# Kernel tuning notes

Hardware: AMD Instinct MI355X
Metric: run time of the kernel (lower is better)

Reference implementation:

```python
import jax, jax.numpy as jnp
import numpy as np

EMBED_DIM = 1024
NUM_HEADS = 16
HEAD_DIM = EMBED_DIM // NUM_HEADS


def setup_inputs() -> dict:
    key = jax.random.key(0)
    k1, k2, k3, k4 = jax.random.split(key, 4)
    x = jax.random.normal(k1, (2, 2048, EMBED_DIM), dtype=jnp.float32)
    # nn.Linear weights: stored as [out, in]; we keep that convention.
    s = 1.0 / np.sqrt(EMBED_DIM)
    w_qkv = jax.random.uniform(k2, (3 * EMBED_DIM, EMBED_DIM), jnp.float32, -s, s)
    w_proj = jax.random.uniform(k3, (EMBED_DIM, EMBED_DIM), jnp.float32, -s, s)
    b_proj = jax.random.uniform(k4, (EMBED_DIM,), jnp.float32, -s, s)
    return {"x": x, "w_qkv": w_qkv, "w_proj": w_proj, "b_proj": b_proj}


def reference(x, w_qkv, w_proj, b_proj):
    B, N, C = x.shape
    H, D = NUM_HEADS, HEAD_DIM
    scale = D ** -0.5
    # qkv: [B, N, 3C] -> [3, B, H, N, D]
    qkv = jnp.einsum('bnc,oc->bno', x, w_qkv)
    qkv = qkv.reshape(B, N, 3, H, D).transpose(2, 0, 3, 1, 4)
    q, k, v = qkv[0] * scale, qkv[1], qkv[2]
    attn = jax.nn.softmax(jnp.einsum('bhnd,bhmd->bhnm', q, k), axis=-1)
    out = jnp.einsum('bhnm,bhmd->bhnd', attn, v)
    out = out.transpose(0, 2, 1, 3).reshape(B, N, C)
    return jnp.einsum('bnc,oc->bno', out, w_proj) + b_proj
```

## Files before the change

### kernel.cpp

```cpp
#include <hip/hip_runtime.h>


constexpr int B_ = 2, N_ = 2048, C_ = 1024, H_ = 16, D_ = 64;
constexpr int M_ = B_ * N_;
constexpr int O3 = 3 * C_;
constexpr int KVB = 64;
constexpr int NTILES = N_ / KVB;

typedef short bf16x8 __attribute__((ext_vector_type(8)));
typedef _Float16 half8 __attribute__((ext_vector_type(8)));
typedef _Float16 half4v __attribute__((ext_vector_type(4)));
typedef float f32x4  __attribute__((ext_vector_type(4)));
typedef float f32x16 __attribute__((ext_vector_type(16)));

__device__ __forceinline__ unsigned short f2bf(float f) {
    unsigned int u = __float_as_uint(f);
    unsigned int r = (u + 0x7FFFu + ((u >> 16) & 1u)) >> 16;
    return (unsigned short)r;
}

__device__ __forceinline__ float fexp2(float x) {
    return __builtin_amdgcn_exp2f(x);
}

__device__ __forceinline__ void async16(const void* g, void* l) {
    __builtin_amdgcn_global_load_lds(
        (const __attribute__((address_space(1))) unsigned int*)g,
        (__attribute__((address_space(3))) unsigned int*)l, 16, 0, 0);
}

constexpr size_t XN  = (size_t)M_ * C_;
constexpr size_t WQN = (size_t)O3 * C_;
constexpr size_t WPN = (size_t)C_ * C_;

__global__ __launch_bounds__(256)
void convert_f16(const float* __restrict__ x, const float* __restrict__ wq,
                 const float* __restrict__ wp, _Float16* __restrict__ dst)
{
    size_t i = ((size_t)blockIdx.x * 256 + threadIdx.x) * 8;
    const float* src;
    size_t off;
    if (i < XN)            { src = x;  off = i; }
    else if (i < XN + WQN) { src = wq; off = i - XN; }
    else                   { src = wp; off = i - XN - WQN; }
    float4 a = *(const float4*)(src + off);
    float4 b = *(const float4*)(src + off + 4);
    half8 h;
    h[0] = (_Float16)a.x; h[1] = (_Float16)a.y; h[2] = (_Float16)a.z; h[3] = (_Float16)a.w;
    h[4] = (_Float16)b.x; h[5] = (_Float16)b.y; h[6] = (_Float16)b.z; h[7] = (_Float16)b.w;
    *(half8*)(dst + i) = h;
}

template<int MODE>
__global__ __launch_bounds__(256)
void gemm128(const _Float16* __restrict__ Ag, const _Float16* __restrict__ Bg,
             unsigned short* __restrict__ Qd, unsigned short* __restrict__ Kd,
             unsigned short* __restrict__ Vt,
             const float* __restrict__ bias, float* __restrict__ Out)
{
    __shared__ __align__(16) unsigned char Ab[2][16384];
    __shared__ __align__(16) unsigned char Bb[2][16384];

    const int t    = threadIdx.x;
    const int lane = t & 63;
    const int w    = t >> 6;
    const int g    = lane >> 4;
    const int c    = lane & 15;
    const int wm   = w >> 1, wn = w & 1;
    const int bm   = blockIdx.y * 128;
    const int bn   = blockIdx.x * 128;
    constexpr int K = C_;

    f32x4 acc[4][4];
    f32x4 zero = {0.f, 0.f, 0.f, 0.f};
    #pragma unroll
    for (int mi = 0; mi < 4; ++mi)
        #pragma unroll
        for (int ni = 0; ni < 4; ++ni) acc[mi][ni] = zero;

    auto stage = [&](int buf, int k0) {
        #pragma unroll
        for (int i = 0; i < 4; ++i) {
            int id  = t + 256 * i;
            int row = id >> 3;
            int p   = id & 7;
            int gs  = p ^ (row & 7);
            async16(Ag + (size_t)(bm + row) * K + k0 + 8 * gs, &Ab[buf][id * 16]);
            async16(Bg + (size_t)(bn + row) * K + k0 + 8 * gs, &Bb[buf][id * 16]);
        }
    };

    stage(0, 0);
    __syncthreads();
    int cur = 0;

    for (int k0 = 0; k0 < K; k0 += 64) {
        if (k0 + 64 < K) stage(cur ^ 1, k0 + 64);

        const unsigned char* Abase = Ab[cur];
        const unsigned char* Bbase = Bb[cur];
        #pragma unroll
        for (int s = 0; s < 2; ++s) {
            half8 af[4], bf[4];
            #pragma unroll
            for (int mi = 0; mi < 4; ++mi) {
                int row = wm * 64 + mi * 16 + c;
                af[mi] = *(const half8*)(Abase + (row * 8 + ((s * 4 + g) ^ (row & 7))) * 16);
            }
            #pragma unroll
            for (int ni = 0; ni < 4; ++ni) {
                int row = wn * 64 + ni * 16 + c;
                bf[ni] = *(const half8*)(Bbase + (row * 8 + ((s * 4 + g) ^ (row & 7))) * 16);
            }
            #pragma unroll
            for (int mi = 0; mi < 4; ++mi)
                #pragma unroll
                for (int ni = 0; ni < 4; ++ni)
                    acc[mi][ni] = __builtin_amdgcn_mfma_f32_16x16x32_f16(af[mi], bf[ni], acc[mi][ni], 0, 0, 0);
        }

        __syncthreads();
        cur ^= 1;
    }

    if constexpr (MODE == 0) {
        constexpr float QSCALE = 0.125f * 1.4426950408889634f;
        const int o0 = bn + wn * 64;
        const int which = o0 >> 10;
        const int h  = (o0 & 1023) >> 6;
        const int m0 = bm + wm * 64;
        const int b  = m0 >> 11;
        const int n0 = m0 & 2047;
        const size_t bh = (size_t)b * H_ + h;
        if (which == 0) {
            unsigned short* base = Qd + (bh * N_) * D_;
            #pragma unroll
            for (int mi = 0; mi < 4; ++mi)
                #pragma unroll
                for (int ni = 0; ni < 4; ++ni)
                    #pragma unroll
                    for (int r = 0; r < 4; ++r)
                        base[(size_t)(n0 + mi * 16 + 4 * g + r) * D_ + ni * 16 + c] =
                            f2bf(acc[mi][ni][r] * QSCALE);
        } else if (which == 1) {
            unsigned short* base = Kd + (bh * N_) * D_;
            #pragma unroll
            for (int mi = 0; mi < 4; ++mi)
                #pragma unroll
                for (int ni = 0; ni < 4; ++ni)
                    #pragma unroll
                    for (int r = 0; r < 4; ++r)
                        base[(size_t)(n0 + mi * 16 + 4 * g + r) * D_ + ni * 16 + c] =
                            f2bf(acc[mi][ni][r]);
        } else {
            unsigned short* base = Vt + (bh * D_) * (size_t)N_;
            #pragma unroll
            for (int mi = 0; mi < 4; ++mi)
                #pragma unroll
                for (int ni = 0; ni < 4; ++ni) {
                    ushort4 v;
                    v.x = f2bf(acc[mi][ni][0]);
                    v.y = f2bf(acc[mi][ni][1]);
                    v.z = f2bf(acc[mi][ni][2]);
                    v.w = f2bf(acc[mi][ni][3]);
                    *(ushort4*)&base[(size_t)(ni * 16 + c) * N_ + n0 + mi * 16 + 4 * g] = v;
                }
        }
    } else {
        const int m0 = bm + wm * 64;
        const int o0 = bn + wn * 64;
        #pragma unroll
        for (int ni = 0; ni < 4; ++ni) {
            float bb = bias[o0 + ni * 16 + c];
            #pragma unroll
            for (int mi = 0; mi < 4; ++mi)
                #pragma unroll
                for (int r = 0; r < 4; ++r)
                    Out[(size_t)(m0 + mi * 16 + 4 * g + r) * C_ + o0 + ni * 16 + c] =
                        acc[mi][ni][r] + bb;
        }
    }
}

__global__ __launch_bounds__(512, 4)
void attn_mfma(const unsigned short* __restrict__ Qd, const unsigned short* __restrict__ Kd,
               const unsigned short* __restrict__ Vt, _Float16* __restrict__ AO)
{
    __shared__ __align__(16) unsigned char Kbuf[2][2][8192];
    __shared__ __align__(16) unsigned char Vbuf[2][2][8192];

    const int t    = threadIdx.x;
    const int lane = t & 63;
    const int w    = t >> 6;
    const int wg   = w >> 2;
    const int wl   = w & 3;
    const int tl   = t & 255;
    const int h    = lane >> 5;
    const int q31  = lane & 31;
    const int qsw  = q31 & 7;

    int flat = blockIdx.x;
    int work = (flat & 7) * 64 + (flat >> 3);
    const int bh = work >> 4;
    const int qt = work & 15;
    const int b  = bh >> 4, hh = bh & 15;
    const int q0 = qt * 128;

    const unsigned short* Kp = Kd + (size_t)bh * N_ * D_;
    const unsigned short* Vp = Vt + (size_t)bh * D_ * N_;

    const unsigned short* qp = Qd + ((size_t)bh * N_ + q0 + wl * 32 + q31) * D_;
    bf16x8 qf[4];
    #pragma unroll
    for (int s = 0; s < 4; ++s)
        qf[s] = *(const bf16x8*)(qp + 16 * s + 8 * h);

    int go[4];
    #pragma unroll
    for (int s = 0; s < 4; ++s) go[s] = ((2 * s + h) ^ qsw) << 4;
    const int row0off = q31 * 128;
    const int row1off = (32 + q31) * 128;

    const int rk = tl >> 3, pk = tl & 7;
    const unsigned char* kSrc = (const unsigned char*)Kp + rk * 128 + ((pk ^ (rk & 7)) << 4);
    const unsigned char* vSrc = (const unsigned char*)Vp + (size_t)rk * (N_ * 2) + ((pk ^ (rk & 7)) << 4);
    unsigned char* kDstA = Kbuf[wg][0] + tl * 16;
    unsigned char* kDstB = Kbuf[wg][1] + tl * 16;
    unsigned char* vDstA = Vbuf[wg][0] + tl * 16;
    unsigned char* vDstB = Vbuf[wg][1] + tl * 16;
    const unsigned char* kb0 = Kbuf[wg][0];
    const unsigned char* kb1 = Kbuf[wg][1];
    const unsigned char* vb0 = Vbuf[wg][0];
    const unsigned char* vb1 = Vbuf[wg][1];

    float l_run = 0.f;
    f32x16 oc0 = 0.f, oc1 = 0.f;

    auto stage = [&](unsigned char* kD, unsigned char* vD, int kt) {
        async16(kSrc + (size_t)kt * 8192, kD);
        async16(kSrc + (size_t)kt * 8192 + 4096, kD + 4096);
        async16(vSrc + (size_t)kt * 128, vD);
        async16(vSrc + 32 * (size_t)(N_ * 2) + (size_t)kt * 128, vD + 4096);
    };

    const int kt0 = wg * 16, ktEnd = kt0 + 16;
    stage(kDstA, vDstA, kt0);
    __syncthreads();

    auto tile_body = [&](const unsigned char* kbase, const unsigned char* vbase,
                         unsigned char* kDstN, unsigned char* vDstN, int ktNext) {
        if (ktNext < ktEnd) stage(kDstN, vDstN, ktNext);

        f32x16 st0 = 0.f, st1 = 0.f;
        const unsigned char* krow0 = kbase + row0off;
        const unsigned char* krow1 = kbase + row1off;
        __builtin_amdgcn_s_setprio(1);
        #pragma unroll
        for (int s = 0; s < 4; ++s) {
            bf16x8 a0 = *(const bf16x8*)(krow0 + go[s]);
            bf16x8 a1 = *(const bf16x8*)(krow1 + go[s]);
            st0 = __builtin_amdgcn_mfma_f32_32x32x16_bf16(a0, qf[s], st0, 0, 0, 0);
            st1 = __builtin_amdgcn_mfma_f32_32x32x16_bf16(a1, qf[s], st1, 0, 0, 0);
        }
        __builtin_amdgcn_s_setprio(0);

        #pragma unroll
        for (int r = 0; r < 16; ++r) {
            st0[r] = fexp2(st0[r]);
            st1[r] = fexp2(st1[r]);
        }

        f32x16 sv = st0 + st1;
        float ts = ((sv[0] + sv[1]) + (sv[2] + sv[3])) + ((sv[4] + sv[5]) + (sv[6] + sv[7]))
                 + ((sv[8] + sv[9]) + (sv[10] + sv[11])) + ((sv[12] + sv[13]) + (sv[14] + sv[15]));
        l_run += ts;

        unsigned int pkd[2][4][2];
        #pragma unroll
        for (int m = 0; m < 4; ++m)
            #pragma unroll
            for (int j = 0; j < 2; ++j) {
                pkd[0][m][j] = __byte_perm(__float_as_uint(st0[4*m + 2*j]),
                                           __float_as_uint(st0[4*m + 2*j + 1]), 0x7632);
                pkd[1][m][j] = __byte_perm(__float_as_uint(st1[4*m + 2*j]),
                                           __float_as_uint(st1[4*m + 2*j + 1]), 0x7632);
            }

        #pragma unroll
        for (int kb = 0; kb < 2; ++kb)
            #pragma unroll
            for (int u = 0; u < 2; ++u)
                #pragma unroll
                for (int j = 0; j < 2; ++j)
                    asm("v_permlane32_swap_b32 %0, %1"
                        : "+v"(pkd[kb][2*u][j]), "+v"(pkd[kb][2*u+1][j]));

        bf16x8 pb[4];
        #pragma unroll
        for (int s = 0; s < 4; ++s) {
            const int kb = s >> 1, u = s & 1;
            union { unsigned int d[4]; bf16x8 v; } uu;
            uu.d[0] = pkd[kb][2*u][0];
            uu.d[1] = pkd[kb][2*u][1];
            uu.d[2] = pkd[kb][2*u+1][0];
            uu.d[3] = pkd[kb][2*u+1][1];
            pb[s] = uu.v;
        }

        const unsigned char* vrow0 = vbase + row0off;
        const unsigned char* vrow1 = vbase + row1off;
        __builtin_amdgcn_s_setprio(1);
        #pragma unroll
        for (int s = 0; s < 4; ++s) {
            bf16x8 va0 = *(const bf16x8*)(vrow0 + go[s]);
            bf16x8 va1 = *(const bf16x8*)(vrow1 + go[s]);
            oc0 = __builtin_amdgcn_mfma_f32_32x32x16_bf16(va0, pb[s], oc0, 0, 0, 0);
            oc1 = __builtin_amdgcn_mfma_f32_32x32x16_bf16(va1, pb[s], oc1, 0, 0, 0);
        }
        __builtin_amdgcn_s_setprio(0);

        __syncthreads();
    };

    #pragma unroll 1
    for (int kt = kt0; kt < ktEnd; kt += 2) {
        tile_body(kb0, vb0, kDstB, vDstB, kt + 1);
        tile_body(kb1, vb1, kDstA, vDstA, kt + 2);
    }

    float* cb = (float*)&Kbuf[0][0][0];
    if (wg == 1) {
        float* s = cb + tl * 36;
        #pragma unroll
        for (int m = 0; m < 4; ++m) {
            f32x4 a, bq;
            #pragma unroll
            for (int i = 0; i < 4; ++i) { a[i] = oc0[4*m + i]; bq[i] = oc1[4*m + i]; }
            *(f32x4*)(s + 4 * m) = a;
            *(f32x4*)(s + 16 + 4 * m) = bq;
        }
        s[32] = l_run;
    }
    __syncthreads();
    if (wg == 0) {
        const float* s  = cb + tl * 36;
        const float* s2 = cb + (tl ^ 32) * 36;
        float l = l_run + __shfl_xor(l_run, 32) + s[32] + s2[32];
        float inv = 1.0f / l;
        const int q = q0 + wl * 32 + q31;
        _Float16* aop = AO + ((size_t)b * N_ + q) * C_ + hh * D_;
        #pragma unroll
        for (int m = 0; m < 4; ++m) {
            half4v o0, o1;
            #pragma unroll
            for (int i = 0; i < 4; ++i) {
                o0[i] = (_Float16)((oc0[4*m + i] + s[4*m + i]) * inv);
                o1[i] = (_Float16)((oc1[4*m + i] + s[16 + 4*m + i]) * inv);
            }
            *(half4v*)(aop + 8 * m + 4 * h) = o0;
            *(half4v*)(aop + 32 + 8 * m + 4 * h) = o1;
        }
    }
}

extern "C" void kernel_launch(void* const* d_in, const int* in_sizes, int n_in,
                              void* d_out, int out_size, void* d_ws, size_t ws_size,
                              hipStream_t stream) {
    const float* x      = (const float*)d_in[0];
    const float* w_qkv  = (const float*)d_in[1];
    const float* w_proj = (const float*)d_in[2];
    const float* b_proj = (const float*)d_in[3];
    float* out = (float*)d_out;

    const size_t hd = (size_t)B_ * H_ * N_ * D_;
    unsigned short* Qd = (unsigned short*)d_ws;
    unsigned short* Kd = Qd + hd;
    unsigned short* Vt = Kd + hd;
    _Float16* AO  = (_Float16*)(Vt + hd);
    _Float16* x16 = AO + hd;
    _Float16* wq16 = x16 + XN;
    _Float16* wp16 = wq16 + WQN;

    convert_f16<<<4096, 256, 0, stream>>>(x, w_qkv, w_proj, x16);
    gemm128<0><<<dim3(O3 / 128, M_ / 128), 256, 0, stream>>>(
        x16, wq16, Qd, Kd, Vt, nullptr, nullptr);
    attn_mfma<<<dim3(512), 512, 0, stream>>>(Qd, Kd, Vt, AO);
    gemm128<1><<<dim3(C_ / 128, M_ / 128), 256, 0, stream>>>(
        AO, wp16, nullptr, nullptr, nullptr, b_proj, out);
}
```

Measured before the change: 115.6 us.

## Software-pipeline QK^T of next KV tile with softmax and PV of current

Restructures the attention inner loop so that the QK^T MFMAs for tile j+1 are issued before the exp, pack and PV work of tile j. K and V staging are split and staggered so that K is prefetched two tiles ahead and V one tile ahead. The aim is to overlap matrix-core work with the transcendental and VALU work and to hide LDS load latency. In exchange, a second set of score accumulators stays live, which raises VGPR pressure and may reduce occupancy.

```diff
diff --git a/kernel.cpp b/kernel.cpp
--- a/kernel.cpp
+++ b/kernel.cpp
@@ -222,12 +222,15 @@
     const int row1off = (32 + q31) * 128;
 
     const int rk = tl >> 3, pk = tl & 7;
-    const unsigned char* kSrc = (const unsigned char*)Kp + rk * 128 + ((pk ^ (rk & 7)) << 4);
-    const unsigned char* vSrc = (const unsigned char*)Vp + (size_t)rk * (N_ * 2) + ((pk ^ (rk & 7)) << 4);
-    unsigned char* kDstA = Kbuf[wg][0] + tl * 16;
-    unsigned char* kDstB = Kbuf[wg][1] + tl * 16;
-    unsigned char* vDstA = Vbuf[wg][0] + tl * 16;
-    unsigned char* vDstB = Vbuf[wg][1] + tl * 16;
+    const int kt0 = wg * 16;
+    const unsigned char* kSrcW = (const unsigned char*)Kp + (size_t)kt0 * 8192
+                               + rk * 128 + ((pk ^ (rk & 7)) << 4);
+    const unsigned char* vSrcW = (const unsigned char*)Vp + (size_t)kt0 * 128
+                               + (size_t)rk * (N_ * 2) + ((pk ^ (rk & 7)) << 4);
+    unsigned char* kDst0 = Kbuf[wg][0] + tl * 16;
+    unsigned char* kDst1 = Kbuf[wg][1] + tl * 16;
+    unsigned char* vDst0 = Vbuf[wg][0] + tl * 16;
+    unsigned char* vDst1 = Vbuf[wg][1] + tl * 16;
     const unsigned char* kb0 = Kbuf[wg][0];
     const unsigned char* kb1 = Kbuf[wg][1];
     const unsigned char* vb0 = Vbuf[wg][0];
@@ -236,22 +239,17 @@
     float l_run = 0.f;
     f32x16 oc0 = 0.f, oc1 = 0.f;
 
-    auto stage = [&](unsigned char* kD, unsigned char* vD, int kt) {
-        async16(kSrc + (size_t)kt * 8192, kD);
-        async16(kSrc + (size_t)kt * 8192 + 4096, kD + 4096);
-        async16(vSrc + (size_t)kt * 128, vD);
-        async16(vSrc + 32 * (size_t)(N_ * 2) + (size_t)kt * 128, vD + 4096);
+    auto stage_k = [&](int j, unsigned char* kD) {
+        async16(kSrcW + (size_t)j * 8192, kD);
+        async16(kSrcW + (size_t)j * 8192 + 4096, kD + 4096);
     };
-
-    const int kt0 = wg * 16, ktEnd = kt0 + 16;
-    stage(kDstA, vDstA, kt0);
-    __syncthreads();
-
-    auto tile_body = [&](const unsigned char* kbase, const unsigned char* vbase,
-                         unsigned char* kDstN, unsigned char* vDstN, int ktNext) {
-        if (ktNext < ktEnd) stage(kDstN, vDstN, ktNext);
-
-        f32x16 st0 = 0.f, st1 = 0.f;
+    auto stage_v = [&](int j, unsigned char* vD) {
+        async16(vSrcW + (size_t)j * 128, vD);
+        async16(vSrcW + 32 * (size_t)(N_ * 2) + (size_t)j * 128, vD + 4096);
+    };
+
+    auto qk = [&](const unsigned char* kbase, f32x16& s0, f32x16& s1) {
+        s0 = 0.f; s1 = 0.f;
         const unsigned char* krow0 = kbase + row0off;
         const unsigned char* krow1 = kbase + row1off;
         __builtin_amdgcn_s_setprio(1);
@@ -259,18 +257,19 @@
         for (int s = 0; s < 4; ++s) {
             bf16x8 a0 = *(const bf16x8*)(krow0 + go[s]);
             bf16x8 a1 = *(const bf16x8*)(krow1 + go[s]);
-            st0 = __builtin_amdgcn_mfma_f32_32x32x16_bf16(a0, qf[s], st0, 0, 0, 0);
-            st1 = __builtin_amdgcn_mfma_f32_32x32x16_bf16(a1, qf[s], st1, 0, 0, 0);
+            s0 = __builtin_amdgcn_mfma_f32_32x32x16_bf16(a0, qf[s], s0, 0, 0, 0);
+            s1 = __builtin_amdgcn_mfma_f32_32x32x16_bf16(a1, qf[s], s1, 0, 0, 0);
         }
         __builtin_amdgcn_s_setprio(0);
-
+    };
+
+    auto softpv = [&](f32x16& s0, f32x16& s1, const unsigned char* vbase) {
         #pragma unroll
         for (int r = 0; r < 16; ++r) {
-            st0[r] = fexp2(st0[r]);
-            st1[r] = fexp2(st1[r]);
-        }
-
-        f32x16 sv = st0 + st1;
+            s0[r] = fexp2(s0[r]);
+            s1[r] = fexp2(s1[r]);
+        }
+        f32x16 sv = s0 + s1;
         float ts = ((sv[0] + sv[1]) + (sv[2] + sv[3])) + ((sv[4] + sv[5]) + (sv[6] + sv[7]))
                  + ((sv[8] + sv[9]) + (sv[10] + sv[11])) + ((sv[12] + sv[13]) + (sv[14] + sv[15]));
         l_run += ts;
@@ -280,12 +279,11 @@
         for (int m = 0; m < 4; ++m)
             #pragma unroll
             for (int j = 0; j < 2; ++j) {
-                pkd[0][m][j] = __byte_perm(__float_as_uint(st0[4*m + 2*j]),
-                                           __float_as_uint(st0[4*m + 2*j + 1]), 0x7632);
-                pkd[1][m][j] = __byte_perm(__float_as_uint(st1[4*m + 2*j]),
-                                           __float_as_uint(st1[4*m + 2*j + 1]), 0x7632);
+                pkd[0][m][j] = __byte_perm(__float_as_uint(s0[4*m + 2*j]),
+                                           __float_as_uint(s0[4*m + 2*j + 1]), 0x7632);
+                pkd[1][m][j] = __byte_perm(__float_as_uint(s1[4*m + 2*j]),
+                                           __float_as_uint(s1[4*m + 2*j + 1]), 0x7632);
             }
-
         #pragma unroll
         for (int kb = 0; kb < 2; ++kb)
             #pragma unroll
@@ -318,14 +316,31 @@
             oc1 = __builtin_amdgcn_mfma_f32_32x32x16_bf16(va1, pb[s], oc1, 0, 0, 0);
         }
         __builtin_amdgcn_s_setprio(0);
-
+    };
+
+    stage_k(0, kDst0);
+    stage_v(0, vDst0);
+    stage_k(1, kDst1);
+    __syncthreads();
+
+    f32x16 sA0, sA1, sB0, sB1;
+    qk(kb0, sA0, sA1);
+
+    #pragma unroll 1
+    for (int j = 0; j < 16; j += 2) {
+        if (j + 2 < 16) stage_k(j + 2, kDst0);
+        stage_v(j + 1, vDst1);
+        qk(kb1, sB0, sB1);
+        softpv(sA0, sA1, vb0);
         __syncthreads();
-    };
-
-    #pragma unroll 1
-    for (int kt = kt0; kt < ktEnd; kt += 2) {
-        tile_body(kb0, vb0, kDstB, vDstB, kt + 1);
-        tile_body(kb1, vb1, kDstA, vDstA, kt + 2);
+
+        if (j + 3 < 16) stage_k(j + 3, kDst1);
+        if (j + 2 < 16) {
+            stage_v(j + 2, vDst0);
+            qk(kb0, sA0, sA1);
+        }
+        softpv(sB0, sB1, vb1);
+        __syncthreads();
     }
 
     float* cb = (float*)&Kbuf[0][0][0];
```

Measured after the change: 253.5 us. 119% more time.
